# Optimization experiments

Measured on AMD Instinct MI355X. Metric: run time of the kernel, lower is better.

## Reference

```python
import jax, jax.numpy as jnp
import numpy as np
from jax import lax

R = 25          # top-k hard attention cutoff
LBP_DAMP = 0.5  # damping factor for loopy BP
LBP_ITER = 5    # number of message-passing rounds
M, C, W, D = 400, 8, 100, 300  # mentions, candidates, ctxt window, vec size
H = 100         # nn_pem_interm_size


def setup_inputs() -> dict:
    key = jax.random.key(0)
    ks = jax.random.split(key, 12)
    ctxt_words = jax.random.randint(ks[0], (M, W), 0, 300000)
    ctxt_words_vec = jax.random.normal(ks[1], (M, W, D), jnp.float32)
    cand_entities = jax.random.randint(ks[2], (M, C), 0, 300000)
    cand_entities_vec = jax.random.normal(ks[3], (M, C, D), jnp.float32)
    p_e_m = -jax.random.uniform(ks[4], (M, C), jnp.float32) * 5.0  # log p(e|m)
    # learned params (A/B/C init to ones in torch; perturb slightly for generality)
    A_linear = 1.0 + 0.02 * jax.random.normal(ks[5], (D,), jnp.float32)
    B_linear = 1.0 + 0.02 * jax.random.normal(ks[6], (D,), jnp.float32)
    C_linear = 1.0 + 0.02 * jax.random.normal(ks[7], (D,), jnp.float32)
    W1 = jax.random.normal(ks[8], (H, 2), jnp.float32) * 0.5
    b1 = jax.random.normal(ks[9], (H,), jnp.float32) * 0.1
    W2 = jax.random.normal(ks[10], (1, H), jnp.float32) * 0.1
    b2 = jax.random.normal(ks[11], (1,), jnp.float32) * 0.1
    return {
        "ctxt_words": ctxt_words, "ctxt_words_vec": ctxt_words_vec,
        "cand_entities": cand_entities, "cand_entities_vec": cand_entities_vec,
        "p_e_m": p_e_m,
        "A_linear": A_linear, "B_linear": B_linear, "C_linear": C_linear,
        "W1": W1, "b1": b1, "W2": W2, "b2": b2,
    }


def _entity_context(ctxt_words_vec, cand_entities_vec, A_linear, B_linear):
    # u_vec[m,c,w] = <A*e_mc, w_mw>
    pre_u = cand_entities_vec * A_linear                       # [M,C,D]
    u_vec = jnp.einsum('mcd,mwd->mcw', pre_u, ctxt_words_vec)  # [M,C,W]
    u = u_vec.max(axis=1)                                      # [M,W]
    top_k = lax.top_k(u, R)[0]                                 # [M,R] sorted desc
    sketch = top_k[:, R - 1][:, None]                          # R-th largest
    minus = u - sketch
    minus = jnp.where(minus > 0, minus, -50.0)  # Threshold(0, -50)
    minus = minus + sketch
    beta = jax.nn.softmax(minus, axis=1)                        # [M,W]
    ctxt_full = jnp.einsum('mwd,mw->md', ctxt_words_vec, beta)  # [M,D]
    scores = jnp.einsum('mcd,md->mc', cand_entities_vec, ctxt_full * B_linear)
    return scores, beta


def reference(ctxt_words, ctxt_words_vec, cand_entities, cand_entities_vec,
              p_e_m, A_linear, B_linear, C_linear, W1, b1, W2, b2):
    scores, beta = _entity_context(ctxt_words_vec, cand_entities_vec,
                                   A_linear, B_linear)          # [M,C]
    # pairwise entity-entity scores
    flat = cand_entities_vec.reshape(M * C, D)
    pairwise = ((flat * C_linear) @ flat.T).reshape(M, C, M, C)  # [M,C,M,C]
    # unary[a,b,m,c] = scores[m,c]
    up = pairwise + scores[None, None, :, :]                     # [M,C,M,C]

    msg = jnp.zeros((M, C, M), jnp.float32)
    # mask[j,:,j] = 0 (self-exclusion)
    mask = 1.0 - jnp.eye(M, dtype=jnp.float32)[:, None, :]       # [M,1,M]
    for _ in range(LBP_ITER):
        crf_old = (1.0 - LBP_DAMP) * jnp.exp(msg)                # [M,C,M]
        s = msg.sum(axis=2)                                      # [M,C]
        new = up + s[None, None, :, :]                           # [M,C,M,C]
        sel = new.max(axis=3)                                    # [M,C,M]
        sel = jax.nn.log_softmax(sel, axis=1)
        sel = sel * mask
        msg = jnp.log(jnp.exp(sel) * LBP_DAMP + crf_old)

    global_message = msg.sum(axis=2)                             # [M,C]
    fgs = jax.nn.log_softmax(scores + global_message, axis=-1)   # [M,C]
    x = jnp.stack([fgs.reshape(-1), p_e_m.reshape(-1)], axis=1)  # [M*C,2]
    x = jax.nn.relu(x @ W1.T + b1)                               # [M*C,H]
    x = x @ W2.T + b2                                            # [M*C,1]
    return x.reshape(M, C)
```

## Files before the change

kernel.cpp:

```cpp
#include <hip/hip_runtime.h>
#include <hip/hip_bf16.h>
#include <math.h>

#define Mm 400
#define Cc 8
#define Ww 100
#define Dd 300
#define Hh 100
#define Rr 25
#define MC 3200
#define KP 320
#define LBP_ITERS 5

typedef _Float16 f16x8 __attribute__((ext_vector_type(8)));
typedef _Float16 f16x4 __attribute__((ext_vector_type(4)));
typedef float f32x4 __attribute__((ext_vector_type(4)));

__device__ __forceinline__ void gload16(const void* g, void* l) {
  __builtin_amdgcn_global_load_lds(
      (const __attribute__((address_space(1))) void*)g,
      (__attribute__((address_space(3))) void*)l, 16, 0, 0);
}

__global__ __launch_bounds__(512) void k_entity(
    const float* __restrict__ ctxt_vec,
    const float* __restrict__ cand_vec,
    const float* __restrict__ A,
    const float* __restrict__ B,
    const float* __restrict__ Cl,
    _Float16* __restrict__ Ah,
    _Float16* __restrict__ Bh,
    float* __restrict__ scores)
{
  const int m = blockIdx.x;
  const int tid = threadIdx.x;
  __shared__ __align__(16) float candA[Cc * 300];
  __shared__ float u_s[Ww];
  __shared__ float beta_s[Ww];
  __shared__ int   idx_s[Ww];
  __shared__ int   cnt_s[2];
  __shared__ __align__(16) float cf_part[6 * 300];
  __shared__ __align__(16) float cfB[304];

  const float* cev = cand_vec + (size_t)m * Cc * Dd;
  const float* cw  = ctxt_vec + (size_t)m * Ww * Dd;

  for (int e = tid; e < 600; e += 512) {
    int c = e / 75, d4 = e - c * 75;
    float4 v = *(const float4*)(cev + c * Dd + d4 * 4);
    float4 a4 = *(const float4*)(A + d4 * 4);
    float4 c4 = *(const float4*)(Cl + d4 * 4);
    *(float4*)&candA[c * 300 + d4 * 4] =
        make_float4(v.x * a4.x, v.y * a4.y, v.z * a4.z, v.w * a4.w);
    size_t go = (size_t)(m * Cc + c) * KP + d4 * 4;
    f16x4 ah = { (_Float16)(v.x * c4.x), (_Float16)(v.y * c4.y),
                 (_Float16)(v.z * c4.z), (_Float16)(v.w * c4.w) };
    f16x4 bh = { (_Float16)v.x, (_Float16)v.y, (_Float16)v.z, (_Float16)v.w };
    *(f16x4*)(Ah + go) = ah;
    *(f16x4*)(Bh + go) = bh;
  }
  if (tid < 40) {
    int r = tid / 5, q = tid - r * 5;
    size_t go = (size_t)(m * Cc + r) * KP + 300 + q * 4;
    f16x4 z = {};
    *(f16x4*)(Ah + go) = z;
    *(f16x4*)(Bh + go) = z;
  }
  __syncthreads();

  {
    const int wv = tid >> 6, l = tid & 63;
    const int cg = l >> 3, d0 = l & 7;
    const float* ca = &candA[cg * 300];
    for (int w = wv; w < Ww; w += 8) {
      const float* row = cw + (size_t)w * Dd;
      float acc = 0.f;
#pragma unroll
      for (int k = 0; k < 10; ++k) {
        int d4 = d0 + k * 8;
        if (d4 < 75) {
          float4 x = *(const float4*)(row + d4 * 4);
          float4 e = *(const float4*)&ca[d4 * 4];
          acc += x.x * e.x + x.y * e.y + x.z * e.z + x.w * e.w;
        }
      }
      acc += __shfl_xor(acc, 1);
      acc += __shfl_xor(acc, 2);
      acc += __shfl_xor(acc, 4);
      acc = fmaxf(acc, __shfl_xor(acc, 8));
      acc = fmaxf(acc, __shfl_xor(acc, 16));
      acc = fmaxf(acc, __shfl_xor(acc, 32));
      if (l == 0) u_s[w] = acc;
    }
  }
  __syncthreads();

  if (tid < 64) {
    float a0 = u_s[tid];
    float a1 = (tid + 64 < Ww) ? u_s[tid + 64] : -1e30f;
    float q0 = a0, q1 = a1, sketch = 0.f;
    for (int r = 0; r < Rr; ++r) {
      float v; int idx;
      if (q1 > q0) { v = q1; idx = tid + 64; } else { v = q0; idx = tid; }
#pragma unroll
      for (int off = 1; off < 64; off <<= 1) {
        float ov = __shfl_xor(v, off);
        int   oi = __shfl_xor(idx, off);
        if (ov > v || (ov == v && oi < idx)) { v = ov; idx = oi; }
      }
      sketch = v;
      if (idx == tid) q0 = -1e30f;
      else if (idx == tid + 64) q1 = -1e30f;
    }
    float m0 = (a0 > sketch) ? a0 : sketch - 50.0f;
    float m1 = (tid + 64 < Ww) ? ((a1 > sketch) ? a1 : sketch - 50.0f) : -1e30f;
    float mx = fmaxf(m0, m1);
#pragma unroll
    for (int off = 1; off < 64; off <<= 1) mx = fmaxf(mx, __shfl_xor(mx, off));
    float e0 = expf(m0 - mx);
    float e1 = (tid + 64 < Ww) ? expf(m1 - mx) : 0.f;
    float s = e0 + e1;
#pragma unroll
    for (int off = 1; off < 64; off <<= 1) s += __shfl_xor(s, off);
    float inv = 1.0f / s;
    beta_s[tid] = e0 * inv;
    if (tid + 64 < Ww) beta_s[tid + 64] = e1 * inv;
  }
  __syncthreads();

  bool sel = false;
  unsigned long long bmask = 0;
  if (tid < 128) {
    sel = (tid < Ww) && (beta_s[tid] > 1e-12f);
    bmask = __ballot(sel);
    if ((tid & 63) == 0) cnt_s[tid >> 6] = (int)__popcll(bmask);
  }
  __syncthreads();
  if (tid < 128 && sel) {
    int lane = tid & 63;
    int base = (tid >> 6) ? cnt_s[0] : 0;
    int pos = base + (int)__popcll(bmask & ((1ull << lane) - 1ull));
    idx_s[pos] = tid;
  }
  __syncthreads();
  const int g = cnt_s[0] + cnt_s[1];

  if (tid < 450) {
    int tg = tid / 75, d4 = tid - tg * 75;
    f32x4 cf = {};
    for (int i = tg; i < g; i += 6) {
      int w = idx_s[i];
      float4 x = *(const float4*)(cw + (size_t)w * Dd + d4 * 4);
      float bw = beta_s[w];
      cf[0] += bw * x.x; cf[1] += bw * x.y; cf[2] += bw * x.z; cf[3] += bw * x.w;
    }
    *(f32x4*)&cf_part[(tg * 75 + d4) * 4] = cf;
  }
  __syncthreads();

  if (tid < 75) {
    f32x4 s4 = *(const f32x4*)&cf_part[tid * 4];
#pragma unroll
    for (int tg = 1; tg < 6; ++tg) s4 += *(const f32x4*)&cf_part[(tg * 75 + tid) * 4];
    float4 b4 = *(const float4*)(B + tid * 4);
    s4[0] *= b4.x; s4[1] *= b4.y; s4[2] *= b4.z; s4[3] *= b4.w;
    *(f32x4*)&cfB[tid * 4] = s4;
  }
  __syncthreads();

  {
    int c = tid >> 6, lane = tid & 63;
    float p = 0.f;
    for (int d4 = lane; d4 < 75; d4 += 64) {
      float4 x = *(const float4*)(cev + (size_t)c * Dd + d4 * 4);
      f32x4 f = *(const f32x4*)&cfB[d4 * 4];
      p += x.x * f[0] + x.y * f[1] + x.z * f[2] + x.w * f[3];
    }
#pragma unroll
    for (int off = 32; off; off >>= 1) p += __shfl_down(p, off);
    if (lane == 0) scores[m * Cc + c] = p;
  }
}

__global__ __launch_bounds__(256) void k_pairwise_mfma(
    const _Float16* __restrict__ Ah,
    const _Float16* __restrict__ Bh,
    _Float16* __restrict__ P)
{
  __shared__ __align__(16) _Float16 Sh[2][128 * 32];
  const int tid = threadIdx.x;
  const int wave = tid >> 6, lane = tid & 63;
  const int wr = wave >> 1, wc = wave & 1;
  const int row0 = blockIdx.y * 128, col0 = blockIdx.x * 128;

  f32x4 acc[4][4] = {};
  const int fr = lane & 15, fq = lane >> 4;
  const int koff = fq * 8;

  for (int kt = 0; kt < KP / 32; ++kt) {
    const int k0 = kt * 32;
#pragma unroll
    for (int i = 0; i < 2; ++i) {
      int e = i * 256 + tid;
      int r = e >> 2;
      int kc = (e & 3) << 3;
      gload16(Ah + (size_t)(row0 + r) * KP + k0 + kc, (char*)Sh[0] + e * 16);
      gload16(Bh + (size_t)(col0 + r) * KP + k0 + kc, (char*)Sh[1] + e * 16);
    }
    __syncthreads();

    f16x8 af[4], bfr[4];
#pragma unroll
    for (int mi = 0; mi < 4; ++mi)
      af[mi] = *(const f16x8*)&Sh[0][(wr * 64 + mi * 16 + fr) * 32 + koff];
#pragma unroll
    for (int ni = 0; ni < 4; ++ni)
      bfr[ni] = *(const f16x8*)&Sh[1][(wc * 64 + ni * 16 + fr) * 32 + koff];
#pragma unroll
    for (int mi = 0; mi < 4; ++mi)
#pragma unroll
      for (int ni = 0; ni < 4; ++ni)
        acc[mi][ni] = __builtin_amdgcn_mfma_f32_16x16x32_f16(
            af[mi], bfr[ni], acc[mi][ni], 0, 0, 0);
    __syncthreads();
  }

  _Float16* wtile = (_Float16*)((char*)Sh + wave * 4096);
#pragma unroll
  for (int h = 0; h < 2; ++h) {
    __syncthreads();
#pragma unroll
    for (int mi2 = 0; mi2 < 2; ++mi2) {
      int mi = h * 2 + mi2;
#pragma unroll
      for (int ni = 0; ni < 4; ++ni)
#pragma unroll
        for (int r = 0; r < 4; ++r)
          wtile[(mi2 * 16 + fq * 4 + r) * 64 + ni * 16 + fr] =
              (_Float16)acc[mi][ni][r];
    }
    __syncthreads();
#pragma unroll
    for (int t = 0; t < 4; ++t) {
      int q = t * 64 + lane;
      int lr = q >> 3, lc8 = (q & 7) * 8;
      f16x8 v = *(const f16x8*)&wtile[lr * 64 + lc8];
      size_t gr = (size_t)(row0 + wr * 64 + h * 32 + lr);
      size_t gc = (size_t)(col0 + wc * 64 + lc8);
      *(f16x8*)(P + gr * MC + gc) = v;
    }
  }
}

__global__ __launch_bounds__(128) void k_lbp(
    const _Float16* __restrict__ P,
    const float* __restrict__ scores,
    const float* __restrict__ pIn,
    float* __restrict__ pOut,
    _Float16* __restrict__ emsg,
    int first)
{
  const int aa = blockIdx.x, q = blockIdx.y;
  const int tid = threadIdx.x;
  __shared__ float red_s[2][Cc];

  float psum[Cc];
#pragma unroll
  for (int b = 0; b < Cc; ++b) psum[b] = 0.f;

  const int m = q * 100 + tid;
  if (tid < 100) {
    const int j8 = m * Cc;
    f32x4 s0 = *(const f32x4*)&scores[j8];
    f32x4 s1 = *(const f32x4*)&scores[j8 + 4];
    if (!first) {
#pragma unroll
      for (int p4 = 0; p4 < 4; ++p4) {
        s0 += *(const f32x4*)&pIn[p4 * MC + j8];
        s1 += *(const f32x4*)&pIn[p4 * MC + j8 + 4];
      }
    }
    float t[Cc];
#pragma unroll
    for (int b = 0; b < Cc; ++b) {
      f16x8 ph = *(const f16x8*)(P + (size_t)(aa * Cc + b) * MC + m * 8);
      float tb = fmaxf(fmaxf((float)ph[0] + s0[0], (float)ph[1] + s0[1]),
                       fmaxf((float)ph[2] + s0[2], (float)ph[3] + s0[3]));
      t[b] = fmaxf(tb, fmaxf(fmaxf((float)ph[4] + s1[0], (float)ph[5] + s1[1]),
                             fmaxf((float)ph[6] + s1[2], (float)ph[7] + s1[3])));
    }
    float mxt = t[0];
#pragma unroll
    for (int b = 1; b < Cc; ++b) mxt = fmaxf(mxt, t[b]);
    float se = 0.f;
#pragma unroll
    for (int b = 0; b < Cc; ++b) { float eb = expf(t[b] - mxt); t[b] = eb; se += eb; }
    float inv_se = 1.0f / se;
    bool self = (m == aa);

    _Float16* ep = emsg + ((size_t)aa * Mm + m) * Cc;
    f16x8 eo;
    if (!first) eo = *(const f16x8*)ep;
    f16x8 en;
#pragma unroll
    for (int b = 0; b < Cc; ++b) {
      float sel_e = self ? 1.0f : t[b] * inv_se;
      float old_e = first ? 1.0f : (float)eo[b];
      float nv = 0.5f * sel_e + 0.5f * old_e;
      en[b] = (_Float16)nv;
      psum[b] += logf(nv);
    }
    *(f16x8*)ep = en;
  }

  const int wave = tid >> 6, lane = tid & 63;
#pragma unroll
  for (int b = 0; b < Cc; ++b)
#pragma unroll
    for (int off = 32; off; off >>= 1) psum[b] += __shfl_down(psum[b], off);
  if (lane == 0)
#pragma unroll
    for (int b = 0; b < Cc; ++b) red_s[wave][b] = psum[b];
  __syncthreads();
  if (tid < Cc)
    pOut[q * MC + aa * Cc + tid] = red_s[0][tid] + red_s[1][tid];
}

__global__ __launch_bounds__(64) void k_final2(
    const float* __restrict__ scores,
    const float* __restrict__ pF,
    const float* __restrict__ pem,
    const float* __restrict__ W1,
    const float* __restrict__ b1,
    const float* __restrict__ W2,
    const float* __restrict__ b2,
    float* __restrict__ out)
{
  int m = blockIdx.x * 64 + threadIdx.x;
  if (m >= Mm) return;
  float f[Cc], pm[Cc];
#pragma unroll
  for (int c = 0; c < Cc; ++c) {
    int j = m * Cc + c;
    f[c] = scores[j] + pF[j] + pF[MC + j] + pF[2 * MC + j] + pF[3 * MC + j];
    pm[c] = pem[j];
  }
  float mx = f[0];
#pragma unroll
  for (int c = 1; c < Cc; ++c) mx = fmaxf(mx, f[c]);
  float se = 0.f;
#pragma unroll
  for (int c = 0; c < Cc; ++c) se += expf(f[c] - mx);
  float lse = mx + logf(se);
  float fgs[Cc], accv[Cc];
  float bb2 = b2[0];
#pragma unroll
  for (int c = 0; c < Cc; ++c) { fgs[c] = f[c] - lse; accv[c] = bb2; }
  for (int h = 0; h < Hh; ++h) {
    float w0 = W1[2 * h], w1 = W1[2 * h + 1], bb = b1[h], w2 = W2[h];
#pragma unroll
    for (int c = 0; c < Cc; ++c)
      accv[c] += w2 * fmaxf(fgs[c] * w0 + pm[c] * w1 + bb, 0.f);
  }
#pragma unroll
  for (int c = 0; c < Cc; ++c) out[m * Cc + c] = accv[c];
}

extern "C" void kernel_launch(void* const* d_in, const int* in_sizes, int n_in,
                              void* d_out, int out_size, void* d_ws, size_t ws_size,
                              hipStream_t stream) {
  const float* ctxt_vec = (const float*)d_in[1];
  const float* cand_vec = (const float*)d_in[3];
  const float* pem      = (const float*)d_in[4];
  const float* A        = (const float*)d_in[5];
  const float* B        = (const float*)d_in[6];
  const float* Cl       = (const float*)d_in[7];
  const float* W1       = (const float*)d_in[8];
  const float* b1       = (const float*)d_in[9];
  const float* W2       = (const float*)d_in[10];
  const float* b2       = (const float*)d_in[11];
  float* out = (float*)d_out;

  char* ws = (char*)d_ws;
  _Float16* P     = (_Float16*)(ws);
  _Float16* Ah    = (_Float16*)(ws + 20480000);
  _Float16* Bh    = (_Float16*)(ws + 20480000 + 2048000);
  _Float16* emsg  = (_Float16*)(ws + 20480000);
  float*   scores = (float*)(ws + 25600000);
  float*   pp     = (float*)(ws + 25612800);

  k_entity<<<Mm, 512, 0, stream>>>(ctxt_vec, cand_vec, A, B, Cl, Ah, Bh, scores);

  dim3 g(MC / 128, MC / 128);
  k_pairwise_mfma<<<g, 256, 0, stream>>>(Ah, Bh, P);

  float* pp0 = pp;
  float* pp1 = pp + 4 * MC;
  for (int it = 0; it < LBP_ITERS; ++it) {
    float* pout = (it & 1) ? pp1 : pp0;
    float* pin  = (it & 1) ? pp0 : pp1;
    k_lbp<<<dim3(Mm, 4), 128, 0, stream>>>(
        P, scores, pin, pout, emsg, it == 0 ? 1 : 0);
  }
  k_final2<<<(Mm + 63) / 64, 64, 0, stream>>>(
      scores, pp0, pem, W1, b1, W2, b2, out);
}
```

Baseline: 106.5 us.

## Split entity kernel into candidate prep, u-score, and score kernels

```diff
diff --git a/kernel.cpp b/kernel.cpp
--- a/kernel.cpp
+++ b/kernel.cpp
@@ -22,19 +22,75 @@
       (__attribute__((address_space(3))) void*)l, 16, 0, 0);
 }
 
-__global__ __launch_bounds__(512) void k_entity(
+__global__ __launch_bounds__(256) void k_candprep(
+    const float* __restrict__ X,
+    const float* __restrict__ Cl,
+    const float* __restrict__ A,
+    _Float16* __restrict__ Ah,
+    _Float16* __restrict__ Bh,
+    float* __restrict__ candA)
+{
+  int idx = blockIdx.x * 256 + threadIdx.x;
+  if (idx >= MC * KP) return;
+  int j = idx / KP, k = idx - j * KP;
+  float x = 0.f, cl = 0.f;
+  if (k < Dd) { x = X[(size_t)j * Dd + k]; cl = Cl[k]; }
+  Bh[idx] = (_Float16)x;
+  Ah[idx] = (_Float16)(x * cl);
+  if (k < Dd) candA[j * Dd + k] = x * A[k];
+}
+
+__global__ __launch_bounds__(64) void k_u(
+    const float* __restrict__ ctxt_vec,
+    const float* __restrict__ candA,
+    float* __restrict__ u)
+{
+  const int wq = blockIdx.x, m = blockIdx.y;
+  const int l = threadIdx.x;
+  const int cg = l >> 3, d0 = l & 7;
+  const float* ca = candA + (size_t)(m * Cc + cg) * Dd;
+
+  f32x4 e[10];
+#pragma unroll
+  for (int k = 0; k < 10; ++k) {
+    int d4 = d0 + k * 8;
+    e[k] = (d4 < 75) ? *(const f32x4*)(ca + d4 * 4) : (f32x4){0.f, 0.f, 0.f, 0.f};
+  }
+
+  const int w0 = wq * 8;
+#pragma unroll
+  for (int i = 0; i < 8; ++i) {
+    int w = w0 + i;
+    if (w >= Ww) break;
+    const float* row = ctxt_vec + ((size_t)m * Ww + w) * Dd;
+    float acc = 0.f;
+#pragma unroll
+    for (int k = 0; k < 10; ++k) {
+      int d4 = d0 + k * 8;
+      if (d4 < 75) {
+        f32x4 x = *(const f32x4*)(row + d4 * 4);
+        acc += x[0] * e[k][0] + x[1] * e[k][1] + x[2] * e[k][2] + x[3] * e[k][3];
+      }
+    }
+    acc += __shfl_xor(acc, 1);
+    acc += __shfl_xor(acc, 2);
+    acc += __shfl_xor(acc, 4);
+    acc = fmaxf(acc, __shfl_xor(acc, 8));
+    acc = fmaxf(acc, __shfl_xor(acc, 16));
+    acc = fmaxf(acc, __shfl_xor(acc, 32));
+    if (l == 0) u[m * 128 + w] = acc;
+  }
+}
+
+__global__ __launch_bounds__(512) void k_escore(
+    const float* __restrict__ u,
     const float* __restrict__ ctxt_vec,
     const float* __restrict__ cand_vec,
-    const float* __restrict__ A,
     const float* __restrict__ B,
-    const float* __restrict__ Cl,
-    _Float16* __restrict__ Ah,
-    _Float16* __restrict__ Bh,
     float* __restrict__ scores)
 {
   const int m = blockIdx.x;
   const int tid = threadIdx.x;
-  __shared__ __align__(16) float candA[Cc * 300];
   __shared__ float u_s[Ww];
   __shared__ float beta_s[Ww];
   __shared__ int   idx_s[Ww];
@@ -42,57 +98,10 @@
   __shared__ __align__(16) float cf_part[6 * 300];
   __shared__ __align__(16) float cfB[304];
 
+  const float* cw  = ctxt_vec + (size_t)m * Ww * Dd;
   const float* cev = cand_vec + (size_t)m * Cc * Dd;
-  const float* cw  = ctxt_vec + (size_t)m * Ww * Dd;
-
-  for (int e = tid; e < 600; e += 512) {
-    int c = e / 75, d4 = e - c * 75;
-    float4 v = *(const float4*)(cev + c * Dd + d4 * 4);
-    float4 a4 = *(const float4*)(A + d4 * 4);
-    float4 c4 = *(const float4*)(Cl + d4 * 4);
-    *(float4*)&candA[c * 300 + d4 * 4] =
-        make_float4(v.x * a4.x, v.y * a4.y, v.z * a4.z, v.w * a4.w);
-    size_t go = (size_t)(m * Cc + c) * KP + d4 * 4;
-    f16x4 ah = { (_Float16)(v.x * c4.x), (_Float16)(v.y * c4.y),
-                 (_Float16)(v.z * c4.z), (_Float16)(v.w * c4.w) };
-    f16x4 bh = { (_Float16)v.x, (_Float16)v.y, (_Float16)v.z, (_Float16)v.w };
-    *(f16x4*)(Ah + go) = ah;
-    *(f16x4*)(Bh + go) = bh;
-  }
-  if (tid < 40) {
-    int r = tid / 5, q = tid - r * 5;
-    size_t go = (size_t)(m * Cc + r) * KP + 300 + q * 4;
-    f16x4 z = {};
-    *(f16x4*)(Ah + go) = z;
-    *(f16x4*)(Bh + go) = z;
-  }
-  __syncthreads();
-
-  {
-    const int wv = tid >> 6, l = tid & 63;
-    const int cg = l >> 3, d0 = l & 7;
-    const float* ca = &candA[cg * 300];
-    for (int w = wv; w < Ww; w += 8) {
-      const float* row = cw + (size_t)w * Dd;
-      float acc = 0.f;
-#pragma unroll
-      for (int k = 0; k < 10; ++k) {
-        int d4 = d0 + k * 8;
-        if (d4 < 75) {
-          float4 x = *(const float4*)(row + d4 * 4);
-          float4 e = *(const float4*)&ca[d4 * 4];
-          acc += x.x * e.x + x.y * e.y + x.z * e.z + x.w * e.w;
-        }
-      }
-      acc += __shfl_xor(acc, 1);
-      acc += __shfl_xor(acc, 2);
-      acc += __shfl_xor(acc, 4);
-      acc = fmaxf(acc, __shfl_xor(acc, 8));
-      acc = fmaxf(acc, __shfl_xor(acc, 16));
-      acc = fmaxf(acc, __shfl_xor(acc, 32));
-      if (l == 0) u_s[w] = acc;
-    }
-  }
+
+  if (tid < Ww) u_s[tid] = u[m * 128 + tid];
   __syncthreads();
 
   if (tid < 64) {
@@ -388,8 +397,13 @@
   _Float16* emsg  = (_Float16*)(ws + 20480000);
   float*   scores = (float*)(ws + 25600000);
   float*   pp     = (float*)(ws + 25612800);
-
-  k_entity<<<Mm, 512, 0, stream>>>(ctxt_vec, cand_vec, A, B, Cl, Ah, Bh, scores);
+  float*   u      = (float*)(ws + 25720000);
+  float*   candA  = (float*)(ws + 25924800);
+
+  k_candprep<<<(MC * KP + 255) / 256, 256, 0, stream>>>(
+      cand_vec, Cl, A, Ah, Bh, candA);
+  k_u<<<dim3(13, Mm), 64, 0, stream>>>(ctxt_vec, candA, u);
+  k_escore<<<Mm, 512, 0, stream>>>(u, ctxt_vec, cand_vec, B, scores);
 
   dim3 g(MC / 128, MC / 128);
   k_pairwise_mfma<<<g, 256, 0, stream>>>(Ah, Bh, P);
```

Measured after the change: 119.0 us. 1.12x slower.
